# Performance work log

Measured on AMD Instinct MI355X. Metric: run time of the kernel, lower is better.

## Reference

```python
import jax, jax.numpy as jnp
import numpy as np

H = 16  # n_heads

def setup_inputs() -> dict:
    key = jax.random.key(0)
    ks = jax.random.split(key, 7)
    B, L, D = 4, 2048, 1024
    s = 0.02
    return {
        "z": jax.random.normal(ks[0], (B, L, D), jnp.float32),
        "connection": jax.random.normal(ks[1], (B, L, D), jnp.float32),
        "Wq": jax.random.normal(ks[2], (2 * D, D), jnp.float32) * s,
        "Wk": jax.random.normal(ks[3], (2 * D, D), jnp.float32) * s,
        "Wv": jax.random.normal(ks[4], (D, D), jnp.float32) * s,
        "Wo": jax.random.normal(ks[5], (D, D), jnp.float32) * s,
        "temp": jnp.float32(1.0),
    }

def reference(z, connection, Wq, Wk, Wv, Wo, temp):
    B, L, D = z.shape
    hd = D // H
    zc = jnp.concatenate([z, connection], axis=-1)          # [B,L,2D]
    Q = (zc @ Wq).reshape(B, L, H, hd).transpose(0, 2, 1, 3)  # [B,H,L,hd]
    K = (zc @ Wk).reshape(B, L, H, hd).transpose(0, 2, 1, 3)
    V = (z @ Wv).reshape(B, L, H, hd).transpose(0, 2, 1, 3)
    scale = (hd ** -0.5) * temp
    scores = jnp.einsum('bhqd,bhkd->bhqk', Q, K) * scale     # [B,H,L,L]
    rel = jax.nn.sigmoid(scores)
    rel_sum = jnp.clip(rel.sum(-1, keepdims=True), 1.0, None)
    out = jnp.einsum('bhqk,bhkd->bhqd', rel, V) / rel_sum
    out = out.transpose(0, 2, 1, 3).reshape(B, L, D)
    return out @ Wo
```

## Files before the change

kernel.cpp:

```cpp
#include <hip/hip_runtime.h>

typedef unsigned short u16;
typedef unsigned int u32;
typedef __bf16 bf16x8 __attribute__((ext_vector_type(8)));
typedef float f32x4 __attribute__((ext_vector_type(4)));

#define DEV static __device__ __forceinline__

DEV void gload16(const void* g, void* l) {
    __builtin_amdgcn_global_load_lds(
        (const __attribute__((address_space(1))) void*)g,
        (__attribute__((address_space(3))) void*)l, 16, 0, 0);
}

DEV void store_c(float* p, float v) { *p = v; }
DEV void store_c(u16* p, float v) { *(__bf16*)p = (__bf16)v; }

DEV int swz(int row, int bytecol) { return row * 128 + (bytecol ^ ((row & 7) << 4)); }

__global__ void pack_zc(const float* __restrict__ z, const float* __restrict__ cn,
                        u16* __restrict__ zc) {
    size_t i = ((size_t)blockIdx.x * blockDim.x + threadIdx.x) * 4;
    size_t t = i >> 11;
    int c = (int)(i & 2047);
    const float* src = (c < 1024) ? (z + t * 1024 + c) : (cn + t * 1024 + (c - 1024));
    float4 v = *reinterpret_cast<const float4*>(src);
    union { __bf16 h[4]; uint2 u; } o;
    o.h[0] = (__bf16)v.x; o.h[1] = (__bf16)v.y;
    o.h[2] = (__bf16)v.z; o.h[3] = (__bf16)v.w;
    *reinterpret_cast<uint2*>(zc + i) = o.u;
}

__global__ void transpose_conv_w(const float* __restrict__ W, u16* __restrict__ WT,
                                 int K, int N) {
    __shared__ float tile[32][33];
    int n0 = blockIdx.x * 32, k0 = blockIdx.y * 32;
    int tx = threadIdx.x, ty = threadIdx.y;
    #pragma unroll
    for (int i = ty; i < 32; i += 8)
        tile[i][tx] = W[(size_t)(k0 + i) * N + n0 + tx];
    __syncthreads();
    #pragma unroll
    for (int i = ty; i < 32; i += 8)
        *(__bf16*)&WT[(size_t)(n0 + i) * K + k0 + tx] = (__bf16)tile[tx][i];
}

__global__ void transpose_v(const u16* __restrict__ Vf, u16* __restrict__ Vt) {
    __shared__ u16 tile[32][33];
    int bh = blockIdx.z; int b = bh >> 4, h = bh & 15;
    int l0 = blockIdx.x * 32, d0 = blockIdx.y * 32;
    int tx = threadIdx.x, ty = threadIdx.y;
    #pragma unroll
    for (int i = ty; i < 32; i += 8)
        tile[i][tx] = Vf[(size_t)(b * 2048 + l0 + i) * 1024 + h * 64 + d0 + tx];
    __syncthreads();
    #pragma unroll
    for (int i = ty; i < 32; i += 8)
        Vt[((size_t)bh * 64 + d0 + i) * 2048 + l0 + tx] = tile[tx][i];
}

template <typename OutT>
__global__ __launch_bounds__(256, 2)
void gemm_bt(const u16* __restrict__ A, const u16* __restrict__ BT,
             OutT* __restrict__ C, int M, int N, int K,
             int lda, int ldb, int ldc) {
    __shared__ u16 As[128 * 64];
    __shared__ u16 Bs[128 * 64];
    const int tid = threadIdx.x;
    const int lane = tid & 63;
    const int wid = tid >> 6;
    const int m0 = blockIdx.x * 128;
    const int n0 = blockIdx.y * 128;
    const int wr = (wid >> 1) * 64;
    const int wc = (wid & 1) * 64;

    f32x4 acc[4][4];
    #pragma unroll
    for (int i = 0; i < 4; ++i)
        #pragma unroll
        for (int j = 0; j < 4; ++j)
            acc[i][j] = f32x4{0.f, 0.f, 0.f, 0.f};

    const int srcoff = ((lane & 7) ^ (lane >> 3)) * 8;
    const int rb = wid * 32 + (lane >> 3);
    const u16* aptr[4]; const u16* bptr[4];
    #pragma unroll
    for (int p = 0; p < 4; ++p) {
        aptr[p] = A  + (size_t)(m0 + rb + p * 8) * lda + srcoff;
        bptr[p] = BT + (size_t)(n0 + rb + p * 8) * ldb + srcoff;
    }

    for (int k0 = 0; k0 < K; k0 += 64) {
        __syncthreads();
        #pragma unroll
        for (int p = 0; p < 4; ++p)
            gload16(aptr[p] + k0, (char*)As + (wid * 4 + p) * 1024);
        #pragma unroll
        for (int p = 0; p < 4; ++p)
            gload16(bptr[p] + k0, (char*)Bs + (wid * 4 + p) * 1024);
        __syncthreads();

        #pragma unroll
        for (int kk = 0; kk < 64; kk += 32) {
            bf16x8 af[4], bfr[4];
            #pragma unroll
            for (int i = 0; i < 4; ++i) {
                int row = wr + i * 16 + (lane & 15);
                af[i] = *reinterpret_cast<const bf16x8*>(
                    reinterpret_cast<const char*>(As) + swz(row, (kk + (lane >> 4) * 8) * 2));
            }
            #pragma unroll
            for (int j = 0; j < 4; ++j) {
                int row = wc + j * 16 + (lane & 15);
                bfr[j] = *reinterpret_cast<const bf16x8*>(
                    reinterpret_cast<const char*>(Bs) + swz(row, (kk + (lane >> 4) * 8) * 2));
            }
            #pragma unroll
            for (int i = 0; i < 4; ++i)
                #pragma unroll
                for (int j = 0; j < 4; ++j)
                    acc[i][j] = __builtin_amdgcn_mfma_f32_16x16x32_bf16(af[i], bfr[j], acc[i][j], 0, 0, 0);
        }
    }

    #pragma unroll
    for (int i = 0; i < 4; ++i)
        #pragma unroll
        for (int j = 0; j < 4; ++j)
            #pragma unroll
            for (int r = 0; r < 4; ++r) {
                int row = m0 + wr + i * 16 + (lane >> 4) * 4 + r;
                int col = n0 + wc + j * 16 + (lane & 15);
                store_c(&C[(size_t)row * ldc + col], acc[i][j][r]);
            }
}

__global__ __launch_bounds__(256, 2)
void attn_kernel(const u16* __restrict__ QKf, const u16* __restrict__ Vt,
                 u16* __restrict__ Oa, const float* __restrict__ temp) {
    constexpr int L = 2048, D = 1024, QKLD = 2048, HD = 64;
    __shared__ u16 Qs[64 * 64];
    __shared__ u16 Ks[64 * 64];
    __shared__ u16 Vs[64 * 64];
    __shared__ u16 Ps[4][16 * 64];

    const int tid = threadIdx.x;
    const int lane = tid & 63;
    const int wid = tid >> 6;
    const int bh = blockIdx.y;
    const int b = bh >> 4, h = bh & 15;
    const int q0 = blockIdx.x * 64;
    const float sneg = -temp[0] * 0.125f * 1.44269504f;

    const u16* Qbase = QKf + (size_t)(b * L) * QKLD + h * HD;
    const u16* Kbase = Qbase + 1024;
    const u16* Vbase = Vt + (size_t)bh * HD * L;

    const int srcoff = ((lane & 7) ^ (lane >> 3)) * 8;
    const int rb = wid * 16 + (lane >> 3);

    #pragma unroll
    for (int p = 0; p < 2; ++p)
        gload16(Qbase + (size_t)(q0 + rb + p * 8) * QKLD + srcoff,
                (char*)Qs + (wid * 2 + p) * 1024);

    const u16* kptr[2]; const u16* vptr[2];
    #pragma unroll
    for (int p = 0; p < 2; ++p) {
        kptr[p] = Kbase + (size_t)(rb + p * 8) * QKLD + srcoff;
        vptr[p] = Vbase + (size_t)(rb + p * 8) * L + srcoff;
    }

    bf16x8 onesf;
    #pragma unroll
    for (int j = 0; j < 8; ++j) onesf[j] = (__bf16)1.0f;

    f32x4 oacc[4];
    #pragma unroll
    for (int j = 0; j < 4; ++j) oacc[j] = f32x4{0.f, 0.f, 0.f, 0.f};
    f32x4 racc = f32x4{0.f, 0.f, 0.f, 0.f};

    for (int k0 = 0; k0 < L; k0 += 64) {
        __syncthreads();
        #pragma unroll
        for (int p = 0; p < 2; ++p)
            gload16(kptr[p] + (size_t)k0 * QKLD, (char*)Ks + (wid * 2 + p) * 1024);
        #pragma unroll
        for (int p = 0; p < 2; ++p)
            gload16(vptr[p] + k0, (char*)Vs + (wid * 2 + p) * 1024);
        __syncthreads();

        f32x4 s[4];
        #pragma unroll
        for (int ct = 0; ct < 4; ++ct) s[ct] = f32x4{0.f, 0.f, 0.f, 0.f};
        #pragma unroll
        for (int kk = 0; kk < 64; kk += 32) {
            int qrow = wid * 16 + (lane & 15);
            bf16x8 aq = *reinterpret_cast<const bf16x8*>(
                reinterpret_cast<const char*>(Qs) + swz(qrow, (kk + (lane >> 4) * 8) * 2));
            #pragma unroll
            for (int ct = 0; ct < 4; ++ct) {
                int krow = ct * 16 + (lane & 15);
                bf16x8 bk = *reinterpret_cast<const bf16x8*>(
                    reinterpret_cast<const char*>(Ks) + swz(krow, (kk + (lane >> 4) * 8) * 2));
                s[ct] = __builtin_amdgcn_mfma_f32_16x16x32_bf16(aq, bk, s[ct], 0, 0, 0);
            }
        }

        #pragma unroll
        for (int ct = 0; ct < 4; ++ct) {
            #pragma unroll
            for (int r = 0; r < 4; ++r) {
                float pv = __builtin_amdgcn_rcpf(1.0f + exp2f(s[ct][r] * sneg));
                int prow = (lane >> 4) * 4 + r;
                *(__bf16*)(reinterpret_cast<char*>(Ps[wid]) +
                    swz(prow, (ct * 16 + (lane & 15)) * 2)) = (__bf16)pv;
            }
        }

        #pragma unroll
        for (int kk = 0; kk < 64; kk += 32) {
            int prow = (lane & 15);
            bf16x8 ap = *reinterpret_cast<const bf16x8*>(
                reinterpret_cast<const char*>(Ps[wid]) + swz(prow, (kk + (lane >> 4) * 8) * 2));
            racc = __builtin_amdgcn_mfma_f32_16x16x32_bf16(ap, onesf, racc, 0, 0, 0);
            #pragma unroll
            for (int ct = 0; ct < 4; ++ct) {
                int vrow = ct * 16 + (lane & 15);
                bf16x8 bv = *reinterpret_cast<const bf16x8*>(
                    reinterpret_cast<const char*>(Vs) + swz(vrow, (kk + (lane >> 4) * 8) * 2));
                oacc[ct] = __builtin_amdgcn_mfma_f32_16x16x32_bf16(ap, bv, oacc[ct], 0, 0, 0);
            }
        }
    }

    float rdiv[4];
    #pragma unroll
    for (int r = 0; r < 4; ++r)
        rdiv[r] = __builtin_amdgcn_rcpf(fmaxf(racc[r], 1.0f));

    #pragma unroll
    for (int ct = 0; ct < 4; ++ct)
        #pragma unroll
        for (int r = 0; r < 4; ++r) {
            int row = q0 + wid * 16 + (lane >> 4) * 4 + r;
            int col = h * HD + ct * 16 + (lane & 15);
            *(__bf16*)&Oa[(size_t)(b * L + row) * D + col] = (__bf16)(oacc[ct][r] * rdiv[r]);
        }
}

extern "C" void kernel_launch(void* const* d_in, const int* in_sizes, int n_in,
                              void* d_out, int out_size, void* d_ws, size_t ws_size,
                              hipStream_t stream) {
    const float* z    = (const float*)d_in[0];
    const float* cn   = (const float*)d_in[1];
    const float* Wq   = (const float*)d_in[2];
    const float* Wk   = (const float*)d_in[3];
    const float* Wv   = (const float*)d_in[4];
    const float* Wo   = (const float*)d_in[5];
    const float* Wo_  = (const float*)d_in[5];
    const float* temp = (const float*)d_in[6];
    (void)Wo_;

    char* ws = (char*)d_ws;
    u16* zc  = (u16*)ws; ws += (size_t)8192 * 2048 * 2;
    u16* WqT = (u16*)ws; ws += (size_t)1024 * 2048 * 2;
    u16* WkT = (u16*)ws; ws += (size_t)1024 * 2048 * 2;
    u16* WvT = (u16*)ws; ws += (size_t)1024 * 1024 * 2;
    u16* WoT = (u16*)ws; ws += (size_t)1024 * 1024 * 2;
    u16* QKf = (u16*)ws; ws += (size_t)8192 * 2048 * 2;
    u16* Vf  = (u16*)ws; ws += (size_t)8192 * 1024 * 2;
    u16* Vt  = zc;
    u16* Oa  = Vf;

    pack_zc<<<16384, 256, 0, stream>>>(z, cn, zc);

    dim3 tb(32, 8);
    transpose_conv_w<<<dim3(32, 64), tb, 0, stream>>>(Wq, WqT, 2048, 1024);
    transpose_conv_w<<<dim3(32, 64), tb, 0, stream>>>(Wk, WkT, 2048, 1024);
    transpose_conv_w<<<dim3(32, 32), tb, 0, stream>>>(Wv, WvT, 1024, 1024);
    transpose_conv_w<<<dim3(32, 32), tb, 0, stream>>>(Wo, WoT, 1024, 1024);

    gemm_bt<u16><<<dim3(64, 16), 256, 0, stream>>>(zc, WqT, QKf, 8192, 2048, 2048, 2048, 2048, 2048);
    gemm_bt<u16><<<dim3(64, 8),  256, 0, stream>>>(zc, WvT, Vf,  8192, 1024, 1024, 2048, 1024, 1024);

    transpose_v<<<dim3(64, 2, 64), tb, 0, stream>>>(Vf, Vt);

    attn_kernel<<<dim3(32, 64), 256, 0, stream>>>(QKf, Vt, Oa, temp);

    gemm_bt<float><<<dim3(64, 8), 256, 0, stream>>>(Oa, WoT, (float*)d_out, 8192, 1024, 1024, 1024, 1024, 1024);
}
```

Measured before the change: 413.8 us.

## Double attention query tile per block and compute transposed scores with packed P stores

The attention kernel now gives each block 128 queries instead of 64, so each wave owns 32 query rows. Every K/V tile loaded into LDS is therefore reused across twice as many queries, and the grid shrinks to half as many blocks. The score MFMA swaps operands (K as A, Q as B), which lets each lane pack four sigmoid probabilities into a single 8-byte LDS store instead of four scalar bf16 stores. In exchange, accumulator register use roughly doubles and there are fewer blocks to fill the CUs.

```diff
diff --git a/kernel.cpp b/kernel.cpp
--- a/kernel.cpp
+++ b/kernel.cpp
@@ -139,17 +139,17 @@
 void attn_kernel(const u16* __restrict__ QKf, const u16* __restrict__ Vt,
                  u16* __restrict__ Oa, const float* __restrict__ temp) {
     constexpr int L = 2048, D = 1024, QKLD = 2048, HD = 64;
-    __shared__ u16 Qs[64 * 64];
+    __shared__ u16 Qs[128 * 64];
     __shared__ u16 Ks[64 * 64];
     __shared__ u16 Vs[64 * 64];
-    __shared__ u16 Ps[4][16 * 64];
+    __shared__ u16 Ps[4][32 * 64];
 
     const int tid = threadIdx.x;
     const int lane = tid & 63;
     const int wid = tid >> 6;
     const int bh = blockIdx.y;
     const int b = bh >> 4, h = bh & 15;
-    const int q0 = blockIdx.x * 64;
+    const int q0 = blockIdx.x * 128;
     const float sneg = -temp[0] * 0.125f * 1.44269504f;
 
     const u16* Qbase = QKf + (size_t)(b * L) * QKLD + h * HD;
@@ -157,13 +157,13 @@
     const u16* Vbase = Vt + (size_t)bh * HD * L;
 
     const int srcoff = ((lane & 7) ^ (lane >> 3)) * 8;
+
+    #pragma unroll
+    for (int p = 0; p < 4; ++p)
+        gload16(Qbase + (size_t)(q0 + wid * 32 + p * 8 + (lane >> 3)) * QKLD + srcoff,
+                (char*)Qs + (wid * 4 + p) * 1024);
+
     const int rb = wid * 16 + (lane >> 3);
-
-    #pragma unroll
-    for (int p = 0; p < 2; ++p)
-        gload16(Qbase + (size_t)(q0 + rb + p * 8) * QKLD + srcoff,
-                (char*)Qs + (wid * 2 + p) * 1024);
-
     const u16* kptr[2]; const u16* vptr[2];
     #pragma unroll
     for (int p = 0; p < 2; ++p) {
@@ -175,10 +175,14 @@
     #pragma unroll
     for (int j = 0; j < 8; ++j) onesf[j] = (__bf16)1.0f;
 
-    f32x4 oacc[4];
-    #pragma unroll
-    for (int j = 0; j < 4; ++j) oacc[j] = f32x4{0.f, 0.f, 0.f, 0.f};
-    f32x4 racc = f32x4{0.f, 0.f, 0.f, 0.f};
+    f32x4 oacc[4][2];
+    #pragma unroll
+    for (int ct = 0; ct < 4; ++ct)
+        #pragma unroll
+        for (int i = 0; i < 2; ++i) oacc[ct][i] = f32x4{0.f, 0.f, 0.f, 0.f};
+    f32x4 racc[2];
+    racc[0] = f32x4{0.f, 0.f, 0.f, 0.f};
+    racc[1] = f32x4{0.f, 0.f, 0.f, 0.f};
 
     for (int k0 = 0; k0 < L; k0 += 64) {
         __syncthreads();
@@ -190,63 +194,88 @@
             gload16(vptr[p] + k0, (char*)Vs + (wid * 2 + p) * 1024);
         __syncthreads();
 
-        f32x4 s[4];
-        #pragma unroll
-        for (int ct = 0; ct < 4; ++ct) s[ct] = f32x4{0.f, 0.f, 0.f, 0.f};
+        f32x4 s[4][2];
+        #pragma unroll
+        for (int ct = 0; ct < 4; ++ct)
+            #pragma unroll
+            for (int i = 0; i < 2; ++i) s[ct][i] = f32x4{0.f, 0.f, 0.f, 0.f};
         #pragma unroll
         for (int kk = 0; kk < 64; kk += 32) {
-            int qrow = wid * 16 + (lane & 15);
-            bf16x8 aq = *reinterpret_cast<const bf16x8*>(
-                reinterpret_cast<const char*>(Qs) + swz(qrow, (kk + (lane >> 4) * 8) * 2));
+            bf16x8 ak[4], bq[2];
             #pragma unroll
             for (int ct = 0; ct < 4; ++ct) {
                 int krow = ct * 16 + (lane & 15);
-                bf16x8 bk = *reinterpret_cast<const bf16x8*>(
+                ak[ct] = *reinterpret_cast<const bf16x8*>(
                     reinterpret_cast<const char*>(Ks) + swz(krow, (kk + (lane >> 4) * 8) * 2));
-                s[ct] = __builtin_amdgcn_mfma_f32_16x16x32_bf16(aq, bk, s[ct], 0, 0, 0);
-            }
+            }
+            #pragma unroll
+            for (int i = 0; i < 2; ++i) {
+                int qrow = wid * 32 + i * 16 + (lane & 15);
+                bq[i] = *reinterpret_cast<const bf16x8*>(
+                    reinterpret_cast<const char*>(Qs) + swz(qrow, (kk + (lane >> 4) * 8) * 2));
+            }
+            #pragma unroll
+            for (int ct = 0; ct < 4; ++ct)
+                #pragma unroll
+                for (int i = 0; i < 2; ++i)
+                    s[ct][i] = __builtin_amdgcn_mfma_f32_16x16x32_bf16(ak[ct], bq[i], s[ct][i], 0, 0, 0);
         }
 
         #pragma unroll
-        for (int ct = 0; ct < 4; ++ct) {
-            #pragma unroll
-            for (int r = 0; r < 4; ++r) {
-                float pv = __builtin_amdgcn_rcpf(1.0f + exp2f(s[ct][r] * sneg));
-                int prow = (lane >> 4) * 4 + r;
-                *(__bf16*)(reinterpret_cast<char*>(Ps[wid]) +
-                    swz(prow, (ct * 16 + (lane & 15)) * 2)) = (__bf16)pv;
+        for (int i = 0; i < 2; ++i) {
+            int prow = i * 16 + (lane & 15);
+            #pragma unroll
+            for (int ct = 0; ct < 4; ++ct) {
+                union { __bf16 hh[4]; uint2 uu; } pk;
+                #pragma unroll
+                for (int r = 0; r < 4; ++r)
+                    pk.hh[r] = (__bf16)__builtin_amdgcn_rcpf(1.0f + exp2f(s[ct][i][r] * sneg));
+                *reinterpret_cast<uint2*>(reinterpret_cast<char*>(Ps[wid]) +
+                    swz(prow, ct * 32 + (lane >> 4) * 8)) = pk.uu;
             }
         }
 
         #pragma unroll
         for (int kk = 0; kk < 64; kk += 32) {
-            int prow = (lane & 15);
-            bf16x8 ap = *reinterpret_cast<const bf16x8*>(
-                reinterpret_cast<const char*>(Ps[wid]) + swz(prow, (kk + (lane >> 4) * 8) * 2));
-            racc = __builtin_amdgcn_mfma_f32_16x16x32_bf16(ap, onesf, racc, 0, 0, 0);
+            bf16x8 ap[2];
+            #pragma unroll
+            for (int i = 0; i < 2; ++i) {
+                int prow = i * 16 + (lane & 15);
+                ap[i] = *reinterpret_cast<const bf16x8*>(
+                    reinterpret_cast<const char*>(Ps[wid]) + swz(prow, (kk + (lane >> 4) * 8) * 2));
+            }
+            racc[0] = __builtin_amdgcn_mfma_f32_16x16x32_bf16(ap[0], onesf, racc[0], 0, 0, 0);
+            racc[1] = __builtin_amdgcn_mfma_f32_16x16x32_bf16(ap[1], onesf, racc[1], 0, 0, 0);
             #pragma unroll
             for (int ct = 0; ct < 4; ++ct) {
                 int vrow = ct * 16 + (lane & 15);
                 bf16x8 bv = *reinterpret_cast<const bf16x8*>(
                     reinterpret_cast<const char*>(Vs) + swz(vrow, (kk + (lane >> 4) * 8) * 2));
-                oacc[ct] = __builtin_amdgcn_mfma_f32_16x16x32_bf16(ap, bv, oacc[ct], 0, 0, 0);
+                #pragma unroll
+                for (int i = 0; i < 2; ++i)
+                    oacc[ct][i] = __builtin_amdgcn_mfma_f32_16x16x32_bf16(ap[i], bv, oacc[ct][i], 0, 0, 0);
             }
         }
     }
 
-    float rdiv[4];
-    #pragma unroll
-    for (int r = 0; r < 4; ++r)
-        rdiv[r] = __builtin_amdgcn_rcpf(fmaxf(racc[r], 1.0f));
+    float rdiv[2][4];
+    #pragma unroll
+    for (int i = 0; i < 2; ++i)
+        #pragma unroll
+        for (int r = 0; r < 4; ++r)
+            rdiv[i][r] = __builtin_amdgcn_rcpf(fmaxf(racc[i][r], 1.0f));
 
     #pragma unroll
     for (int ct = 0; ct < 4; ++ct)
         #pragma unroll
-        for (int r = 0; r < 4; ++r) {
-            int row = q0 + wid * 16 + (lane >> 4) * 4 + r;
-            int col = h * HD + ct * 16 + (lane & 15);
-            *(__bf16*)&Oa[(size_t)(b * L + row) * D + col] = (__bf16)(oacc[ct][r] * rdiv[r]);
-        }
+        for (int i = 0; i < 2; ++i)
+            #pragma unroll
+            for (int r = 0; r < 4; ++r) {
+                int row = q0 + wid * 32 + i * 16 + (lane >> 4) * 4 + r;
+                int col = h * HD + ct * 16 + (lane & 15);
+                *(__bf16*)&Oa[(size_t)(b * L + row) * D + col] =
+                    (__bf16)(oacc[ct][i][r] * rdiv[i][r]);
+            }
 }
 
 extern "C" void kernel_launch(void* const* d_in, const int* in_sizes, int n_in,
@@ -258,9 +287,7 @@
     const float* Wk   = (const float*)d_in[3];
     const float* Wv   = (const float*)d_in[4];
     const float* Wo   = (const float*)d_in[5];
-    const float* Wo_  = (const float*)d_in[5];
     const float* temp = (const float*)d_in[6];
-    (void)Wo_;
 
     char* ws = (char*)d_ws;
     u16* zc  = (u16*)ws; ws += (size_t)8192 * 2048 * 2;
@@ -286,7 +313,7 @@
 
     transpose_v<<<dim3(64, 2, 64), tb, 0, stream>>>(Vf, Vt);
 
-    attn_kernel<<<dim3(32, 64), 256, 0, stream>>>(QKf, Vt, Oa, temp);
+    attn_kernel<<<dim3(16, 64), 256, 0, stream>>>(QKf, Vt, Oa, temp);
 
     gemm_bt<float><<<dim3(64, 8), 256, 0, stream>>>(Oa, WoT, (float*)d_out, 8192, 1024, 1024, 1024, 1024, 1024);
 }
```

New measurement: 414.1 us. About the same (+0.1%).
